# Kernel optimization log

Hardware: AMD Instinct MI355X
Metric: run time of the kernel (lower is better)

## Reference

```python
import jax, jax.numpy as jnp
import numpy as np
from jax import lax

BS, T, DF = 256, 128, 40
HID, UNITS = 64, 64


def _lstm_seq(x, W, U, b):
    """Keras-style LSTM (gate order i,f,c,o), return_sequences=True, eval mode.
    x: (B,T,Din); W: (Din,4H); U: (H,4H); b: (4H,) -> (B,T,H)."""
    B = x.shape[0]
    H = U.shape[0]
    h0 = jnp.zeros((B, H), x.dtype)
    c0 = jnp.zeros((B, H), x.dtype)

    def step(carry, xt):
        h, c = carry
        z = xt @ W + h @ U + b
        i, f, g, o = jnp.split(z, 4, axis=-1)
        i = jax.nn.sigmoid(i)
        f = jax.nn.sigmoid(f)
        g = jnp.tanh(g)
        o = jax.nn.sigmoid(o)
        c = f * c + i * g
        h = o * jnp.tanh(c)
        return (h, c), h

    _, hs = lax.scan(step, (h0, c0), jnp.swapaxes(x, 0, 1))  # (T,B,H)
    return jnp.swapaxes(hs, 0, 1)


def _norm_abs(a, axis=1):
    aa = jnp.abs(a) + 1e-8
    return aa / jnp.sum(aa, axis=axis, keepdims=True)


def setup_inputs() -> dict:
    key = jax.random.key(0)
    ks = jax.random.split(key, 10)
    s = lambda k, shape, fan: (jax.random.normal(k, shape, jnp.float32) * np.float32(1.0 / np.sqrt(fan)))
    return {
        "x": jax.random.normal(ks[0], (BS, T, DF), jnp.float32),
        "W0": s(ks[1], (DF, 4 * HID), DF),
        "U0": s(ks[2], (HID, 4 * HID), HID),
        "b0": jnp.zeros((4 * HID,), jnp.float32),
        "W1": s(ks[3], (HID, 4 * UNITS), HID),
        "U1": s(ks[4], (UNITS, 4 * UNITS), UNITS),
        "b1": jnp.zeros((4 * UNITS,), jnp.float32),
        "kernel": s(ks[5], (1, 1, DF, UNITS), DF),       # feature projection kernel
        "bias": s(ks[6], (1, 1, DF, UNITS), DF),         # feature projection bias
        "beta_w": s(ks[7], (1, T, 1), T),                # unnormalised time-agg weights
    }


def reference(x, W0, U0, b0, W1, U1, b1, kernel, bias, beta_w):
    # Stacked LSTM encoder (hidden layer + output layer, return_sequences=True)
    h = _lstm_seq(x, W0, U0, b0)                 # (B,T,HID)
    latent_reps = _lstm_seq(h, W1, U1, b1)       # (B,T,UNITS)

    # FeatTimeAttention: per-(b,t) feature projections (activation='linear')
    fp = x[..., None] * kernel + bias            # (B,T,DF,UNITS)

    # OLS alpha estimation: G = X^T X (DF,DF), XTy = X^T y (DF,)
    G = jnp.einsum('btdu,bteu->btde', fp, fp)    # (B,T,DF,DF)
    G_inv = jnp.linalg.inv(G)
    XTy = jnp.einsum('btdu,btu->btd', fp, latent_reps)
    alpha = jnp.einsum('btde,bte->btd', G_inv, XTy)  # (B,T,DF)

    # Approximate latent states and time-weighted aggregation
    o_hat = jnp.einsum('btd,btdu->btu', alpha, fp)   # (B,T,UNITS)
    beta = _norm_abs(beta_w, axis=1)                 # (1,T,1)
    z = jnp.sum(o_hat * beta, axis=1)                # (B,UNITS)
    return z
```

## Files before the change

kernel.cpp:

```cpp
#include <hip/hip_runtime.h>
#include <math.h>

#define DEVI __device__ __forceinline__

DEVI float rlane(float v, int l) {
    return __builtin_bit_cast(float, __builtin_amdgcn_readlane(__builtin_bit_cast(int, v), l));
}
DEVI float sigf(float v) { return 1.0f / (1.0f + __expf(-v)); }
DEVI float tanh_f(float v) {
    v = fminf(fmaxf(v, -15.0f), 15.0f);
    float e = __expf(2.0f * v);
    return (e - 1.0f) / (e + 1.0f);
}

__global__ void precompute_kernel(const float* __restrict__ Kg, const float* __restrict__ Bg,
                                  const float* __restrict__ betaw,
                                  float4* __restrict__ Qg, float4* __restrict__ KBg,
                                  float* __restrict__ beta) {
    int job = blockIdx.x * 256 + threadIdx.x;
    if (job < 1600) {
        int d = job / 40, e = job - d * 40;
        const float* kd = Kg + d * 64;
        const float* ke = Kg + e * 64;
        const float* bd = Bg + d * 64;
        const float* be = Bg + e * 64;
        float kk = 0, kbT = 0, kbr = 0, bb = 0;
        for (int u = 0; u < 64; ++u) {
            kk  = fmaf(kd[u], ke[u], kk);
            kbT = fmaf(ke[u], bd[u], kbT);
            kbr = fmaf(kd[u], be[u], kbr);
            bb  = fmaf(bd[u], be[u], bb);
        }
        Qg[job] = make_float4(kk, kbT, kbr, bb);
    } else if (job < 2880) {
        int j2 = job - 1600;
        int d = j2 >> 5, q = j2 & 31;
        KBg[j2] = make_float4(Kg[d * 64 + 2 * q], Kg[d * 64 + 2 * q + 1],
                              Bg[d * 64 + 2 * q], Bg[d * 64 + 2 * q + 1]);
    }
    if (blockIdx.x == 0) {
        int tid = threadIdx.x;
        __shared__ float red[256];
        float av = (tid < 128) ? (fabsf(betaw[tid]) + 1e-8f) : 0.0f;
        red[tid] = av;
        __syncthreads();
        for (int s = 128; s > 0; s >>= 1) {
            if (tid < s) red[tid] += red[tid + s];
            __syncthreads();
        }
        float tot = red[0];
        if (tid < 128) beta[tid] = av / tot;
    }
}

__global__ __launch_bounds__(512)
void lstm2_kernel(const float* __restrict__ x,
                  const float* __restrict__ W0, const float* __restrict__ U0,
                  const float* __restrict__ b0,
                  const float* __restrict__ W1, const float* __restrict__ U1,
                  const float* __restrict__ b1,
                  float* __restrict__ y) {
    int b = blockIdx.x;
    int tid = threadIdx.x;
    int j = tid & 255;
    int lane = tid & 63;
    int grp = __builtin_amdgcn_readfirstlane(tid) >> 8;

    float wcol[64];
    float ucol[64];
    float bj;
    if (grp == 0) {
#pragma unroll
        for (int d = 0; d < 40; ++d) wcol[d] = W0[d * 256 + j];
#pragma unroll
        for (int k = 0; k < 64; ++k) ucol[k] = U0[k * 256 + j];
        bj = b0[j];
    } else {
#pragma unroll
        for (int k = 0; k < 64; ++k) wcol[k] = W1[k * 256 + j];
#pragma unroll
        for (int k = 0; k < 64; ++k) ucol[k] = U1[k * 256 + j];
        bj = b1[j];
    }

    __shared__ float x_lds[128 * 40];
    __shared__ float a_lds[2][512];
    __shared__ float h1buf[2][64];
    const float4* xg = (const float4*)(x + (size_t)b * 128 * 40);
    float4* xl = (float4*)x_lds;
    for (int i = tid; i < 128 * 40 / 4; i += 512) xl[i] = xg[i];
    if (tid < 128) h1buf[tid >> 6][tid & 63] = 0.0f;
    float c = 0.0f;
    float h = 0.0f;
    __syncthreads();

    int li = (lane < 40) ? lane : 0;
#pragma unroll 1
    for (int s = 0; s < 130; ++s) {
        int p = s & 1;
        float a0 = bj, a1 = 0.0f, a2 = 0.0f, a3 = 0.0f;
        if (grp == 0) {
            if (s < 128) {
                float xv = x_lds[s * 40 + li];
#pragma unroll
                for (int d = 0; d < 40; d += 4) {
                    a0 = fmaf(rlane(xv, d), wcol[d], a0);
                    a1 = fmaf(rlane(xv, d + 1), wcol[d + 1], a1);
                    a2 = fmaf(rlane(xv, d + 2), wcol[d + 2], a2);
                    a3 = fmaf(rlane(xv, d + 3), wcol[d + 3], a3);
                }
#pragma unroll
                for (int k = 0; k < 64; k += 4) {
                    a0 = fmaf(rlane(h, k), ucol[k], a0);
                    a1 = fmaf(rlane(h, k + 1), ucol[k + 1], a1);
                    a2 = fmaf(rlane(h, k + 2), ucol[k + 2], a2);
                    a3 = fmaf(rlane(h, k + 3), ucol[k + 3], a3);
                }
            }
        } else {
            if (s >= 2) {
                float h1x = h1buf[p][lane];
#pragma unroll
                for (int k = 0; k < 64; k += 4) {
                    a0 = fmaf(rlane(h1x, k), wcol[k], a0);
                    a1 = fmaf(rlane(h1x, k + 1), wcol[k + 1], a1);
                    a2 = fmaf(rlane(h1x, k + 2), wcol[k + 2], a2);
                    a3 = fmaf(rlane(h1x, k + 3), wcol[k + 3], a3);
                }
#pragma unroll
                for (int k = 0; k < 64; k += 4) {
                    a0 = fmaf(rlane(h, k), ucol[k], a0);
                    a1 = fmaf(rlane(h, k + 1), ucol[k + 1], a1);
                    a2 = fmaf(rlane(h, k + 2), ucol[k + 2], a2);
                    a3 = fmaf(rlane(h, k + 3), ucol[k + 3], a3);
                }
            }
        }
        float z = (a0 + a1) + (a2 + a3);
        int g = (tid >> 6) & 3;
        float a = (g == 2) ? tanh_f(z) : sigf(z);
        a_lds[p][tid] = a;
        __syncthreads();
        if (grp == 0) {
            if (s < 128) {
                const float* pp = &a_lds[p][0];
                float iv = pp[lane], fv = pp[lane + 64];
                float gv = pp[lane + 128], ov = pp[lane + 192];
                c = fmaf(fv, c, iv * gv);
                h = ov * tanh_f(c);
                if (tid < 64) h1buf[p][lane] = h;
            }
        } else {
            if (s >= 2) {
                const float* pp = &a_lds[p][256];
                float iv = pp[lane], fv = pp[lane + 64];
                float gv = pp[lane + 128], ov = pp[lane + 192];
                c = fmaf(fv, c, iv * gv);
                h = ov * tanh_f(c);
                if (tid < 320) y[((size_t)b * 128 + (s - 2)) * 64 + lane] = h;
            }
        }
    }
}

__launch_bounds__(256)
__global__ void attn_kernel(const float* __restrict__ xin, const float* __restrict__ yin,
                            const float4* __restrict__ Qg, const float4* __restrict__ KBg,
                            const float* __restrict__ betap, float* __restrict__ zpart) {
    __shared__ float4 sQ4[40 * 41];
    __shared__ float4 sKB4[40 * 33];
    __shared__ float redW[4][64];
    __shared__ float redA[4][64];
    __shared__ float wsf[64];
    __shared__ float asf[64];
    int tid = threadIdx.x;
    for (int i = tid; i < 1600; i += 256) {
        int d = i / 40, e = i - d * 40;
        sQ4[d * 41 + e] = Qg[i];
    }
    for (int i = tid; i < 1280; i += 256) {
        int d = i >> 5, q = i & 31;
        sKB4[d * 33 + q] = KBg[i];
    }
    __syncthreads();

    int b = blockIdx.x >> 2;
    int qq = blockIdx.x & 3;
    int wv = tid >> 6;
    int lane = tid & 63;
    int rl0 = (lane < 40) ? lane : 39;
    const float4* Qrow = sQ4 + rl0 * 41;
    const float4* KBrow = sKB4 + rl0 * 33;

    float wsx = 0.f, wsy = 0.f, asx = 0.f, asy = 0.f;
    int su = __builtin_amdgcn_readfirstlane(wv);
    int t0u = qq * 32 + su * 8;
    size_t bt0u = (size_t)b * 128 + t0u;

#pragma unroll 1
    for (int it = 0; it < 4; ++it) {
        const float* yr0 = yin + (bt0u + 2 * it) * 64;
        const float* yr1 = yr0 + 64;
        const float* xr0 = xin + (bt0u + 2 * it) * 40;
        const float* xr1 = xr0 + 40;
        float btx = betap[t0u + 2 * it];
        float bty = betap[t0u + 2 * it + 1];

        float xvx = xr0[rl0];
        float xvy = xr1[rl0];
        if (lane >= 40) { xvx = 0.f; xvy = 0.f; }

        float t1ax = 0.f, t1ay = 0.f, t1bx = 0.f, t1by = 0.f;
        float t2ax = 0.f, t2ay = 0.f, t2bx = 0.f, t2by = 0.f;
#pragma unroll
        for (int q = 0; q < 32; ++q) {
            float4 kb = KBrow[q];
            float s0x = yr0[2 * q], s1x = yr0[2 * q + 1];
            float s0y = yr1[2 * q], s1y = yr1[2 * q + 1];
            t1ax = fmaf(kb.x, s0x, t1ax); t1ay = fmaf(kb.x, s0y, t1ay);
            t1bx = fmaf(kb.y, s1x, t1bx); t1by = fmaf(kb.y, s1y, t1by);
            t2ax = fmaf(kb.z, s0x, t2ax); t2ay = fmaf(kb.z, s0y, t2ay);
            t2bx = fmaf(kb.w, s1x, t2bx); t2by = fmaf(kb.w, s1y, t2by);
        }

        float Ax[41], Ay[41];
        Ax[40] = fmaf(xvx, t1ax + t1bx, t2ax + t2bx);
        Ay[40] = fmaf(xvy, t1ay + t1by, t2ay + t2by);
#pragma unroll
        for (int e = 0; e < 40; ++e) {
            float4 q4 = Qrow[e];
            float sxx = xr0[e];
            float sxy = xr1[e];
            Ax[e] = fmaf(sxx, fmaf(xvx, q4.x, q4.y), fmaf(xvx, q4.z, q4.w));
            Ay[e] = fmaf(sxy, fmaf(xvy, q4.x, q4.y), fmaf(xvy, q4.z, q4.w));
        }

        float rplx = 0.f, rply = 0.f;
#pragma unroll
        for (int k = 0; k < 40; ++k) {
            float rpx = __builtin_amdgcn_rcpf(rlane(Ax[k], k));
            float rpy = __builtin_amdgcn_rcpf(rlane(Ay[k], k));
            bool ne = (lane != k);
            float mx = ne ? Ax[k] * rpx : 0.f;
            float my = ne ? Ay[k] * rpy : 0.f;
            rplx = ne ? rplx : rpx;
            rply = ne ? rply : rpy;
#pragma unroll
            for (int jj = k + 1; jj <= 40; ++jj) {
                Ax[jj] = fmaf(-mx, rlane(Ax[jj], k), Ax[jj]);
                Ay[jj] = fmaf(-my, rlane(Ay[jj], k), Ay[jj]);
            }
        }
        float alphax = Ax[40] * rplx;
        float alphay = Ay[40] * rply;

        wsx = fmaf(btx, alphax * xvx, wsx);
        wsy = fmaf(bty, alphay * xvy, wsy);
        asx = fmaf(btx, alphax, asx);
        asy = fmaf(bty, alphay, asy);
    }

    redW[wv][lane] = wsx + wsy;
    redA[wv][lane] = asx + asy;
    __syncthreads();
    if (tid < 64) {
        wsf[tid] = (redW[0][tid] + redW[1][tid]) + (redW[2][tid] + redW[3][tid]);
    } else if (tid < 128) {
        int d = tid - 64;
        asf[d] = (redA[0][d] + redA[1][d]) + (redA[2][d] + redA[3][d]);
    }
    __syncthreads();
    if (tid < 64) {
        const float* KBf = (const float*)sKB4;
        int u = tid;
        int off = ((u >> 1) << 2) + (u & 1);
        float z = 0.0f;
#pragma unroll
        for (int d = 0; d < 40; ++d) {
            float kv = KBf[d * 132 + off];
            float bv = KBf[d * 132 + off + 2];
            z = fmaf(wsf[d], kv, z);
            z = fmaf(asf[d], bv, z);
        }
        zpart[((size_t)b * 4 + qq) * 64 + u] = z;
    }
}

__global__ void reduce_kernel(const float* __restrict__ zpart, float* __restrict__ out) {
    int idx = blockIdx.x * 256 + threadIdx.x;
    int b = idx >> 6, u = idx & 63;
    const float* zp = zpart + (size_t)b * 4 * 64 + u;
    out[idx] = (zp[0] + zp[64]) + (zp[128] + zp[192]);
}

extern "C" void kernel_launch(void* const* d_in, const int* in_sizes, int n_in,
                              void* d_out, int out_size, void* d_ws, size_t ws_size,
                              hipStream_t stream) {
    const float* x  = (const float*)d_in[0];
    const float* W0 = (const float*)d_in[1];
    const float* U0 = (const float*)d_in[2];
    const float* b0 = (const float*)d_in[3];
    const float* W1 = (const float*)d_in[4];
    const float* U1 = (const float*)d_in[5];
    const float* b1 = (const float*)d_in[6];
    const float* Kg = (const float*)d_in[7];
    const float* Bg = (const float*)d_in[8];
    const float* bw = (const float*)d_in[9];
    float* out = (float*)d_out;

    float* y     = (float*)d_ws;
    float4* Qg   = (float4*)(y + 256 * 128 * 64);
    float4* KBg  = Qg + 1600;
    float* beta  = (float*)(KBg + 1280);
    float* zpart = beta + 128;

    precompute_kernel<<<12, 256, 0, stream>>>(Kg, Bg, bw, Qg, KBg, beta);
    lstm2_kernel<<<256, 512, 0, stream>>>(x, W0, U0, b0, W1, U1, b1, y);
    attn_kernel<<<1024, 256, 0, stream>>>(x, y, Qg, KBg, beta, zpart);
    reduce_kernel<<<64, 256, 0, stream>>>(zpart, out);
}
```

Baseline: 355.5 us.

## Replace Gauss-Jordan solve with forward elimination plus back substitution; atomically reduce output

Result: no change. 352.6 us (-0.8%).

```diff
diff --git a/kernel.cpp b/kernel.cpp
--- a/kernel.cpp
+++ b/kernel.cpp
@@ -166,7 +166,7 @@
 __launch_bounds__(256)
 __global__ void attn_kernel(const float* __restrict__ xin, const float* __restrict__ yin,
                             const float4* __restrict__ Qg, const float4* __restrict__ KBg,
-                            const float* __restrict__ betap, float* __restrict__ zpart) {
+                            const float* __restrict__ betap, float* __restrict__ out) {
     __shared__ float4 sQ4[40 * 41];
     __shared__ float4 sKB4[40 * 33];
     __shared__ float redW[4][64];
@@ -235,24 +235,32 @@
             Ay[e] = fmaf(sxy, fmaf(xvy, q4.x, q4.y), fmaf(xvy, q4.z, q4.w));
         }
 
-        float rplx = 0.f, rply = 0.f;
 #pragma unroll
         for (int k = 0; k < 40; ++k) {
             float rpx = __builtin_amdgcn_rcpf(rlane(Ax[k], k));
             float rpy = __builtin_amdgcn_rcpf(rlane(Ay[k], k));
-            bool ne = (lane != k);
-            float mx = ne ? Ax[k] * rpx : 0.f;
-            float my = ne ? Ay[k] * rpy : 0.f;
-            rplx = ne ? rplx : rpx;
-            rply = ne ? rply : rpy;
+            bool gt = (lane > k);
+            float mx = gt ? Ax[k] * rpx : 0.f;
+            float my = gt ? Ay[k] * rpy : 0.f;
 #pragma unroll
             for (int jj = k + 1; jj <= 40; ++jj) {
                 Ax[jj] = fmaf(-mx, rlane(Ax[jj], k), Ax[jj]);
                 Ay[jj] = fmaf(-my, rlane(Ay[jj], k), Ay[jj]);
             }
         }
-        float alphax = Ax[40] * rplx;
-        float alphay = Ay[40] * rply;
+
+        float accx = Ax[40], accy = Ay[40];
+        float alphax = 0.f, alphay = 0.f;
+#pragma unroll
+        for (int k = 39; k >= 0; --k) {
+            float xk = rlane(accx, k) * __builtin_amdgcn_rcpf(rlane(Ax[k], k));
+            float yk = rlane(accy, k) * __builtin_amdgcn_rcpf(rlane(Ay[k], k));
+            bool eq = (lane == k);
+            alphax = eq ? xk : alphax;
+            alphay = eq ? yk : alphay;
+            accx = fmaf(-xk, Ax[k], accx);
+            accy = fmaf(-yk, Ay[k], accy);
+        }
 
         wsx = fmaf(btx, alphax * xvx, wsx);
         wsy = fmaf(bty, alphay * xvy, wsy);
@@ -282,15 +290,8 @@
             z = fmaf(wsf[d], kv, z);
             z = fmaf(asf[d], bv, z);
         }
-        zpart[((size_t)b * 4 + qq) * 64 + u] = z;
-    }
-}
-
-__global__ void reduce_kernel(const float* __restrict__ zpart, float* __restrict__ out) {
-    int idx = blockIdx.x * 256 + threadIdx.x;
-    int b = idx >> 6, u = idx & 63;
-    const float* zp = zpart + (size_t)b * 4 * 64 + u;
-    out[idx] = (zp[0] + zp[64]) + (zp[128] + zp[192]);
+        atomicAdd(&out[b * 64 + u], z);
+    }
 }
 
 extern "C" void kernel_launch(void* const* d_in, const int* in_sizes, int n_in,
@@ -312,10 +313,9 @@
     float4* Qg   = (float4*)(y + 256 * 128 * 64);
     float4* KBg  = Qg + 1600;
     float* beta  = (float*)(KBg + 1280);
-    float* zpart = beta + 128;
-
+
+    hipMemsetAsync(d_out, 0, (size_t)out_size * sizeof(float), stream);
     precompute_kernel<<<12, 256, 0, stream>>>(Kg, Bg, bw, Qg, KBg, beta);
     lstm2_kernel<<<256, 512, 0, stream>>>(x, W0, U0, b0, W1, U1, b1, y);
-    attn_kernel<<<1024, 256, 0, stream>>>(x, y, Qg, KBg, beta, zpart);
-    reduce_kernel<<<64, 256, 0, stream>>>(zpart, out);
-}
+    attn_kernel<<<1024, 256, 0, stream>>>(x, y, Qg, KBg, beta, out);
+}
```
